# Kernel tuning notes

Hardware: AMD Instinct MI355X
Metric: run time of the kernel (lower is better)

## Reference

```python
import jax, jax.numpy as jnp
import numpy as np
import math

L, D, H, B, NT = 4, 512, 8, 128, 512
D_HID = int(D * 4.0 / 3.0)  # 682; linear0 outputs 2*D_HID for reglu
EPS = 1e-5


def layer_norm(x, g, b):
    mu = jnp.mean(x, axis=-1, keepdims=True)
    var = jnp.var(x, axis=-1, keepdims=True)
    return (x - mu) * jax.lax.rsqrt(var + EPS) * g + b


def mha(x_q, x_kv, Wq, bq, Wk, bk, Wv, bv, Wo, bo):
    q = x_q @ Wq.T + bq
    k = x_kv @ Wk.T + bk
    v = x_kv @ Wv.T + bv
    Bq, Sq, _ = q.shape
    Sk = k.shape[1]
    dh = D // H
    q = q.reshape(Bq, Sq, H, dh).transpose(0, 2, 1, 3)  # [B,H,Sq,dh]
    k = k.reshape(Bq, Sk, H, dh).transpose(0, 2, 1, 3)
    v = v.reshape(Bq, Sk, H, dh).transpose(0, 2, 1, 3)
    dots = jnp.einsum('bhqd,bhkd->bhqk', q, k) / math.sqrt(dh)
    attn = jax.nn.softmax(dots, axis=-1)
    o = jnp.einsum('bhqk,bhkd->bhqd', attn, v)
    o = o.transpose(0, 2, 1, 3).reshape(Bq, Sq, D)
    return o @ Wo.T + bo


def reglu(x):
    a, b = jnp.split(x, 2, axis=-1)
    return a * jax.nn.relu(b)


def setup_inputs() -> dict:
    key = jax.random.key(0)
    ks = iter(jax.random.split(key, 32))
    s = 0.02
    return {
        'x_num': jax.random.normal(next(ks), (B, NT, D), jnp.float32),
        'cls_w': jax.random.normal(next(ks), (1, D), jnp.float32) * s,
        'Wq': jax.random.normal(next(ks), (L, D, D), jnp.float32) * s,
        'bq': jnp.zeros((L, D), jnp.float32),
        'Wk': jax.random.normal(next(ks), (L, D, D), jnp.float32) * s,
        'bk': jnp.zeros((L, D), jnp.float32),
        'Wv': jax.random.normal(next(ks), (L, D, D), jnp.float32) * s,
        'bv': jnp.zeros((L, D), jnp.float32),
        'Wo': jax.random.normal(next(ks), (L, D, D), jnp.float32) * s,
        'bo': jnp.zeros((L, D), jnp.float32),
        'l0_w': jax.random.normal(next(ks), (L, 2 * D_HID, D), jnp.float32) * s,
        'l0_b': jnp.zeros((L, 2 * D_HID), jnp.float32),
        'l1_w': jax.random.normal(next(ks), (L, D, D_HID), jnp.float32) * s,
        'l1_b': jnp.zeros((L, D), jnp.float32),
        'n0_g': jnp.ones((L - 1, D), jnp.float32),
        'n0_b': jnp.zeros((L - 1, D), jnp.float32),
        'n1_g': jnp.ones((L, D), jnp.float32),
        'n1_b': jnp.zeros((L, D), jnp.float32),
        'ln_g': jnp.ones((D,), jnp.float32),
        'ln_b': jnp.zeros((D,), jnp.float32),
        'head_w': jax.random.normal(next(ks), (1, D), jnp.float32) * s,
        'head_b': jnp.zeros((1,), jnp.float32),
    }


def reference(x_num, cls_w, Wq, bq, Wk, bk, Wv, bv, Wo, bo,
              l0_w, l0_b, l1_w, l1_b, n0_g, n0_b, n1_g, n1_b,
              ln_g, ln_b, head_w, head_b):
    # prepend CLS token: cls_weight broadcast over batch
    x_cls = jnp.broadcast_to(cls_w[None], (x_num.shape[0], 1, D))
    x = jnp.concatenate([x_cls, x_num], axis=1)  # [B, NT+1, D]
    for i in range(L):
        is_last = i + 1 == L
        # attention block (prenormalization; layer 0 has no norm0)
        xr = layer_norm(x, n0_g[i - 1], n0_b[i - 1]) if i > 0 else x
        x_q = xr[:, :1] if is_last else xr  # last layer: query only CLS
        xr = mha(x_q, xr, Wq[i], bq[i], Wk[i], bk[i], Wv[i], bv[i], Wo[i], bo[i])
        if is_last:
            x = x[:, :1]
        x = x + xr
        # FFN block with reglu
        xr = layer_norm(x, n1_g[i], n1_b[i])
        xr = reglu(xr @ l0_w[i].T + l0_b[i])
        xr = xr @ l1_w[i].T + l1_b[i]
        x = x + xr
    x = x[:, 0]  # CLS representation [B, D]
    x = layer_norm(x, ln_g, ln_b)
    x = jax.nn.relu(x)
    x = x @ head_w.T + head_b
    return x.squeeze(-1)  # [B]
```

## Files before the change

kernel.cpp:

```cpp
#include <hip/hip_runtime.h>
#include <stdint.h>

typedef __attribute__((ext_vector_type(4))) float f32x4;
typedef __attribute__((ext_vector_type(8))) short short8;
typedef __attribute__((ext_vector_type(8))) _Float16 half8;

#define DMODEL 512
#define SEQ 513
#define BATCH 128
#define NROWS (BATCH*SEQ)
#define DHID 682
#define DHID2 1364
#define HP 768
#define QKVS 1536
#define KVB 64
#define NKT 9
#define QSF 0.1803368801111244f

__device__ __forceinline__ float h2f(ushort u){ return (float)__builtin_bit_cast(_Float16, u); }
__device__ __forceinline__ ushort f2h(float f){ return __builtin_bit_cast(ushort, (_Float16)f); }
__device__ __forceinline__ uint pk2h(float a, float b){
  return __builtin_bit_cast(uint, __builtin_amdgcn_cvt_pkrtz(a, b));
}
__device__ __forceinline__ void gload16(const void* g, void* lds){
  __builtin_amdgcn_global_load_lds((const __attribute__((address_space(1))) void*)g,
                                   (__attribute__((address_space(3))) void*)lds, 16, 0, 0);
}
__device__ __forceinline__ int xcd_wg(int orig, int nwg){
  const int q = nwg >> 3, r = nwg & 7;
  const int xcd = orig & 7, idx = orig >> 3;
  return (xcd < r) ? (xcd*(q+1) + idx) : (r*(q+1) + (xcd-r)*q + idx);
}

template<int EPI>
__global__ __launch_bounds__(256,3) void gemm_bt(
    const ushort* __restrict__ A, const ushort* __restrict__ W,
    const float* __restrict__ bias, ushort* __restrict__ Cb, float* __restrict__ Cf,
    int K, int ldc, int gx, int nwg)
{
  __shared__ char lds[32768];
  const int t = threadIdx.x, lane = t & 63, w = t >> 6;
  const int fr = lane & 15, g = lane >> 4;
  const int l7 = lane & 7, l8 = lane >> 3;
  const int wg = xcd_wg(blockIdx.x, nwg);
  const int row0 = (wg / gx) << 7;
  const int col0 = (wg % gx) << 7;
  const int wr = (w >> 1) << 6, wc = (w & 1) << 6;

  const int chunkoff = (l7 ^ l8) << 3;
  const ushort* Ag = A + (size_t)(row0 + w*8 + l8) * K + chunkoff;
  const ushort* Wg = W + (size_t)(col0 + w*8 + l8) * K + chunkoff;

  f32x4 acc[4][4] = {};

  for (int k0 = 0; k0 < K; k0 += 64) {
    __syncthreads();
#pragma unroll
    for (int p = 0; p < 4; ++p) {
      gload16(Ag + (size_t)(p*32)*K + k0, lds + p*4096 + w*1024);
      gload16(Wg + (size_t)(p*32)*K + k0, lds + 16384 + p*4096 + w*1024);
    }
    __syncthreads();
#pragma unroll
    for (int ks = 0; ks < 2; ++ks) {
      half8 af[4], wf[4];
#pragma unroll
      for (int m = 0; m < 4; ++m) {
        const int row = wr + m*16 + fr;
        af[m] = *(const half8*)(lds + row*128 + (((g + ks*4) ^ (fr & 7)) << 4));
      }
#pragma unroll
      for (int n = 0; n < 4; ++n) {
        const int row = wc + n*16 + fr;
        wf[n] = *(const half8*)(lds + 16384 + row*128 + (((g + ks*4) ^ (fr & 7)) << 4));
      }
#pragma unroll
      for (int m = 0; m < 4; ++m)
#pragma unroll
        for (int n = 0; n < 4; ++n)
          acc[m][n] = __builtin_amdgcn_mfma_f32_16x16x32_f16(af[m], wf[n], acc[m][n], 0, 0, 0);
    }
  }

  const int r0 = (lane >> 4) << 2;
#pragma unroll
  for (int m = 0; m < 4; ++m) {
    const int rg = row0 + wr + m*16 + r0;
#pragma unroll
    for (int n = 0; n < 4; ++n) {
      const int cg = col0 + wc + n*16 + fr;
      const float bi = bias[cg];
      if (EPI == 0) {
#pragma unroll
        for (int r = 0; r < 4; ++r)
          Cb[(size_t)(rg + r)*ldc + cg] = f2h(acc[m][n][r] + bi);
      } else {
#pragma unroll
        for (int r = 0; r < 4; ++r) {
          const size_t ix = (size_t)(rg + r)*ldc + cg;
          Cf[ix] += acc[m][n][r] + bi;
        }
      }
    }
  }
}

__global__ __launch_bounds__(256,2) void gemm_res_ln(
    const ushort* __restrict__ A, const ushort* __restrict__ W,
    const float* __restrict__ bias, float* __restrict__ x,
    const float* __restrict__ gamma, const float* __restrict__ beta,
    ushort* __restrict__ xb, int K)
{
  __shared__ char lds[73728];
  const int t = threadIdx.x, lane = t & 63, w = t >> 6;
  const int fr = lane & 15, g = lane >> 4;
  const int l7 = lane & 7, l8 = lane >> 3;
  const int row0 = blockIdx.x << 6;

  const int chunkoff = (l7 ^ l8) << 3;
  const ushort* Ag = A + (size_t)(row0 + w*8 + l8) * K + chunkoff;
  const ushort* Wg = W + (size_t)(w*8 + l8) * K + chunkoff;

  f32x4 acc[4][8] = {};

  for (int k0 = 0; k0 < K; k0 += 64) {
    __syncthreads();
    gload16(Ag + k0,                 lds + w*1024);
    gload16(Ag + (size_t)32*K + k0,  lds + 4096 + w*1024);
#pragma unroll
    for (int p = 0; p < 16; ++p)
      gload16(Wg + (size_t)(p*32)*K + k0, lds + 8192 + p*4096 + w*1024);
    __syncthreads();
#pragma unroll
    for (int ks = 0; ks < 2; ++ks) {
      half8 af[4], wf[8];
#pragma unroll
      for (int m = 0; m < 4; ++m) {
        const int row = m*16 + fr;
        af[m] = *(const half8*)(lds + row*128 + (((g + ks*4) ^ (fr & 7)) << 4));
      }
#pragma unroll
      for (int n = 0; n < 8; ++n) {
        const int row = (w << 7) + n*16 + fr;
        wf[n] = *(const half8*)(lds + 8192 + row*128 + (((g + ks*4) ^ (fr & 7)) << 4));
      }
#pragma unroll
      for (int m = 0; m < 4; ++m)
#pragma unroll
        for (int n = 0; n < 8; ++n)
          acc[m][n] = __builtin_amdgcn_mfma_f32_16x16x32_f16(af[m], wf[n], acc[m][n], 0, 0, 0);
    }
  }

  ushort* fb16   = (ushort*)lds;
  float2* redrow = (float2*)(lds + 66560);
  float*  gb     = (float*)(lds + 67072);

  __syncthreads();
#pragma unroll
  for (int n = 0; n < 8; ++n) {
    const int cg = (w << 7) + n*16 + fr;
    const float bi = bias[cg];
#pragma unroll
    for (int m = 0; m < 4; ++m)
#pragma unroll
      for (int r = 0; r < 4; ++r)
        fb16[(m*16 + g*4 + r)*520 + cg] = f2h(acc[m][n][r] + bi);
  }
  if (t < 128) *(f32x4*)&gb[t*4]            = *(const f32x4*)&gamma[t*4];
  else         *(f32x4*)&gb[512 + (t-128)*4] = *(const f32x4*)&beta[(t-128)*4];
  __syncthreads();

  const int q = t & 15;
  const int rbase = t >> 4;
#pragma unroll
  for (int rr = 0; rr < 4; ++rr) {
    const int row = rr*16 + rbase;
    const size_t xrow = (size_t)(row0 + row)*DMODEL;
    float ps = 0.f, pss = 0.f;
#pragma unroll
    for (int j = 0; j < 8; ++j) {
      const int c = q*4 + j*64;
      const uint2 pk = *(const uint2*)&fb16[row*520 + c];
      f32x4 v;
      v[0] = h2f((ushort)(pk.x & 0xffffu)); v[1] = h2f((ushort)(pk.x >> 16));
      v[2] = h2f((ushort)(pk.y & 0xffffu)); v[3] = h2f((ushort)(pk.y >> 16));
      const f32x4 xo = *(const f32x4*)&x[xrow + c];
      v += xo;
      *(f32x4*)&x[xrow + c] = v;
      uint2 opk; opk.x = pk2h(v[0], v[1]); opk.y = pk2h(v[2], v[3]);
      *(uint2*)&fb16[row*520 + c] = opk;
      ps  += v[0]+v[1]+v[2]+v[3];
      pss += v[0]*v[0]+v[1]*v[1]+v[2]*v[2]+v[3]*v[3];
    }
#pragma unroll
    for (int mask = 1; mask <= 8; mask <<= 1) {
      ps  += __shfl_xor(ps,  mask);
      pss += __shfl_xor(pss, mask);
    }
    if (q == 0) redrow[row] = float2{ps, pss};
  }
  __syncthreads();
#pragma unroll
  for (int rr = 0; rr < 4; ++rr) {
    const int row = rr*16 + rbase;
    const float2 sr = redrow[row];
    const float mu = sr.x * (1.f/512.f);
    const float rstd = rsqrtf(sr.y*(1.f/512.f) - mu*mu + 1e-5f);
    const size_t xbrow = (size_t)(row0 + row)*DMODEL;
#pragma unroll
    for (int j = 0; j < 8; ++j) {
      const int c = q*4 + j*64;
      const uint2 pk = *(const uint2*)&fb16[row*520 + c];
      f32x4 v;
      v[0] = h2f((ushort)(pk.x & 0xffffu)); v[1] = h2f((ushort)(pk.x >> 16));
      v[2] = h2f((ushort)(pk.y & 0xffffu)); v[3] = h2f((ushort)(pk.y >> 16));
      const f32x4 ga = *(const f32x4*)&gb[c];
      const f32x4 be = *(const f32x4*)&gb[512 + c];
      f32x4 o_;
#pragma unroll
      for (int e = 0; e < 4; ++e) o_[e] = (v[e] - mu)*rstd*ga[e] + be[e];
      uint2 u; u.x = pk2h(o_[0], o_[1]); u.y = pk2h(o_[2], o_[3]);
      *(uint2*)&xb[xbrow + c] = u;
    }
  }
}

__global__ __launch_bounds__(256,2) void gemm_ffn(
    const ushort* __restrict__ A, const ushort* __restrict__ Wa, const ushort* __restrict__ Wb,
    const float* __restrict__ ba, const float* __restrict__ bb, ushort* __restrict__ H,
    int K, int ldc, int gx, int nwg)
{
  __shared__ char lds[49152];
  const int t = threadIdx.x, lane = t & 63, w = t >> 6;
  const int fr = lane & 15, g = lane >> 4;
  const int l7 = lane & 7, l8 = lane >> 3;
  const int wg = xcd_wg(blockIdx.x, nwg);
  const int row0 = (wg / gx) << 7;
  const int col0 = (wg % gx) << 7;
  const int wr = (w >> 1) << 6, wc = (w & 1) << 6;

  const int chunkoff = (l7 ^ l8) << 3;
  const ushort* Ag  = A  + (size_t)(row0 + w*8 + l8) * K + chunkoff;
  const ushort* WaG = Wa + (size_t)(col0 + w*8 + l8) * K + chunkoff;
  const ushort* WbG = Wb + (size_t)(col0 + w*8 + l8) * K + chunkoff;

  f32x4 aa[4][4] = {}, ab[4][4] = {};

  for (int k0 = 0; k0 < K; k0 += 64) {
    __syncthreads();
#pragma unroll
    for (int p = 0; p < 4; ++p) {
      gload16(Ag  + (size_t)(p*32)*K + k0, lds + p*4096 + w*1024);
      gload16(WaG + (size_t)(p*32)*K + k0, lds + 16384 + p*4096 + w*1024);
      gload16(WbG + (size_t)(p*32)*K + k0, lds + 32768 + p*4096 + w*1024);
    }
    __syncthreads();
#pragma unroll
    for (int ks = 0; ks < 2; ++ks) {
      half8 af[4], wa[4], wb[4];
#pragma unroll
      for (int m = 0; m < 4; ++m) {
        const int row = wr + m*16 + fr;
        af[m] = *(const half8*)(lds + row*128 + (((g + ks*4) ^ (fr & 7)) << 4));
      }
#pragma unroll
      for (int n = 0; n < 4; ++n) {
        const int row = wc + n*16 + fr;
        const int off = row*128 + (((g + ks*4) ^ (fr & 7)) << 4);
        wa[n] = *(const half8*)(lds + 16384 + off);
        wb[n] = *(const half8*)(lds + 32768 + off);
      }
#pragma unroll
      for (int m = 0; m < 4; ++m)
#pragma unroll
        for (int n = 0; n < 4; ++n) {
          aa[m][n] = __builtin_amdgcn_mfma_f32_16x16x32_f16(af[m], wa[n], aa[m][n], 0, 0, 0);
          ab[m][n] = __builtin_amdgcn_mfma_f32_16x16x32_f16(af[m], wb[n], ab[m][n], 0, 0, 0);
        }
    }
  }

  const int r0 = (lane >> 4) << 2;
#pragma unroll
  for (int m = 0; m < 4; ++m) {
    const int rg = row0 + wr + m*16 + r0;
#pragma unroll
    for (int n = 0; n < 4; ++n) {
      const int cg = col0 + wc + n*16 + fr;
      const float bav = ba[cg], bbv = bb[cg];
#pragma unroll
      for (int r = 0; r < 4; ++r) {
        const float av = aa[m][n][r] + bav;
        const float bv = ab[m][n][r] + bbv;
        H[(size_t)(rg + r)*ldc + cg] = f2h(av * fmaxf(bv, 0.f));
      }
    }
  }
}

__global__ __launch_bounds__(256,4) void attn_fused(
    const ushort* __restrict__ qkv, ushort* __restrict__ o)
{
  __shared__ char lds[40960];
  const int t = threadIdx.x;

  if (blockIdx.x >= 4096) {
    const int bh = blockIdx.x - 4096;
    const int b = bh >> 3, h = bh & 7;
    float* sc   = (float*)lds;
    float* qsh  = (float*)(lds + 2112);
    float* red  = (float*)(lds + 2368);
    float* osum = (float*)(lds + 2432);
    const ushort* k = qkv + 512;
    const ushort* v = qkv + 1024;
    const ushort* qb2 = qkv + (size_t)512*QKVS;
    if (t < 64) qsh[t] = h2f(qb2[(size_t)b*SEQ*QKVS + h*64 + t]);
    __syncthreads();
    for (int key = t; key < SEQ; key += 256) {
      const ushort* kr = k + ((size_t)b*SEQ + key)*QKVS + h*64;
      float s = 0.f;
#pragma unroll 8
      for (int d = 0; d < 64; ++d) s += qsh[d]*h2f(kr[d]);
      sc[key] = s;
    }
    __syncthreads();
    float lm = -1e30f;
    for (int key = t; key < SEQ; key += 256) lm = fmaxf(lm, sc[key]);
#pragma unroll
    for (int mask=1; mask<64; mask<<=1) lm = fmaxf(lm, __shfl_xor(lm, mask));
    if ((t&63)==0) red[t>>6] = lm;
    __syncthreads();
    const float mx = fmaxf(fmaxf(red[0],red[1]), fmaxf(red[2],red[3]));
    float ls = 0.f;
    for (int key = t; key < SEQ; key += 256){ float pp = exp2f(sc[key]-mx); sc[key]=pp; ls += pp; }
#pragma unroll
    for (int mask=1; mask<64; mask<<=1) ls += __shfl_xor(ls, mask);
    if ((t&63)==0) red[4 + (t>>6)] = ls;
    __syncthreads();
    const float ssum = red[4]+red[5]+red[6]+red[7];
    const int d = t & 63, kc = t >> 6;
    float op = 0.f;
    for (int key = kc; key < SEQ; key += 4)
      op += sc[key] * h2f(v[((size_t)b*SEQ + key)*QKVS + h*64 + d]);
    osum[t] = op;
    __syncthreads();
    if (t < 64) {
      const float oo = (osum[t]+osum[64+t]+osum[128+t]+osum[192+t]) / ssum;
      o[((size_t)b*SEQ + 512)*DMODEL + h*64 + t] = f2h(oo);
    }
    return;
  }

  const int bid = blockIdx.x;
  const int sw = (bid & 7)*512 + (bid >> 3);
  const int qt = sw & 3;
  const int hb = sw >> 2;
  const int h = hb & 7, b = hb >> 3;
  const int lane = t & 63, w = t >> 6;
  const int fr = lane & 15, g = lane >> 4, gq4 = g << 2;
  const size_t rowB = (size_t)b * SEQ;
  const ushort* q = qkv;
  const ushort* k = qkv + 512;
  const ushort* v = qkv + 1024;

  char* const Ks  = lds;
  char* const Vs  = lds + 8192;
  char* const VTs = lds + 16384;
  char* const pb  = lds + 24576 + w*4096;

  const int qr0 = qt*128 + w*32;

  half8 qf[2][2];
#pragma unroll
  for (int nq = 0; nq < 2; ++nq) {
    const int qrow = qr0 + nq*16 + fr;
#pragma unroll
    for (int kk = 0; kk < 2; ++kk)
      qf[nq][kk] = *(const half8*)&q[(rowB + qrow)*QKVS + h*64 + kk*32 + g*8];
  }

  f32x4 accO[2][4] = {};
  float mrun[2] = {-1e30f, -1e30f};
  float lrun[2] = {0.f, 0.f};

  const int l8 = lane >> 3, l7 = lane & 7;
  const int chunk = l7 ^ l8;
  auto STAGE = [&](int kt2) {
#pragma unroll
    for (int i = 0; i < 2; ++i) {
      const int row = i*32 + (w<<3) + l8;
      const int keyg = min(kt2*KVB + row, 512);
      const size_t gsrc = (rowB + keyg)*QKVS + h*64 + chunk*8;
      gload16(k + gsrc, Ks + i*4096 + w*1024);
      gload16(v + gsrc, Vs + i*4096 + w*1024);
    }
  };

  const int db  = (lane & 7) | ((w & 1) << 3);
  const int kbq = l8 | ((w & 2) << 2);
  const int d0 = db << 2, key0 = kbq << 2;

  STAGE(0);

  for (int kt = 0; kt < NKT; ++kt) {
    __syncthreads();

    f32x4 sc4[4][2] = {};
    __builtin_amdgcn_s_setprio(1);
#pragma unroll
    for (int kk = 0; kk < 2; ++kk) {
      half8 kf[4];
#pragma unroll
      for (int mk = 0; mk < 4; ++mk) {
        const int row = mk*16 + fr;
        kf[mk] = *(const half8*)(Ks + row*128 + ((kk*64 + g*16) ^ ((fr&7)<<4)));
      }
#pragma unroll
      for (int mk = 0; mk < 4; ++mk)
#pragma unroll
        for (int nq = 0; nq < 2; ++nq)
          sc4[mk][nq] = __builtin_amdgcn_mfma_f32_16x16x32_f16(kf[mk], qf[nq][kk], sc4[mk][nq], 0, 0, 0);
    }
    __builtin_amdgcn_s_setprio(0);

    {
      uint2 a[4];
#pragma unroll
      for (int i = 0; i < 4; ++i) {
        const int row = key0 + i;
        a[i] = *(const uint2*)(Vs + row*128 + ((d0*2) ^ ((row&7)<<4)));
      }
      uint2 bb[4];
      bb[0].x = (a[0].x & 0xffffu) | (a[1].x << 16);
      bb[0].y = (a[2].x & 0xffffu) | (a[3].x << 16);
      bb[1].x = (a[0].x >> 16) | (a[1].x & 0xffff0000u);
      bb[1].y = (a[2].x >> 16) | (a[3].x & 0xffff0000u);
      bb[2].x = (a[0].y & 0xffffu) | (a[1].y << 16);
      bb[2].y = (a[2].y & 0xffffu) | (a[3].y << 16);
      bb[3].x = (a[0].y >> 16) | (a[1].y & 0xffff0000u);
      bb[3].y = (a[2].y >> 16) | (a[3].y & 0xffff0000u);
#pragma unroll
      for (int j = 0; j < 4; ++j) {
        const int drow = d0 + j;
        *(uint2*)(VTs + drow*128 + ((key0*2) ^ ((drow&7)<<4))) = bb[j];
      }
    }

    if (kt == NKT-1) {
#pragma unroll
      for (int mk = 0; mk < 4; ++mk)
#pragma unroll
        for (int r = 0; r < 4; ++r)
          if (mk + gq4 + r) { sc4[mk][0][r] = -1e30f; sc4[mk][1][r] = -1e30f; }
    }

    __syncthreads();

    if (kt+1 < NKT) STAGE(kt+1);

    float al2[2];
    bool resc[2];
#pragma unroll
    for (int nq = 0; nq < 2; ++nq) {
      float tm = sc4[0][nq][0];
#pragma unroll
      for (int mk = 0; mk < 4; ++mk)
#pragma unroll
        for (int r = 0; r < 4; ++r) tm = fmaxf(tm, sc4[mk][nq][r]);
      tm = fmaxf(tm, __shfl_xor(tm, 16));
      tm = fmaxf(tm, __shfl_xor(tm, 32));
      float mref;
      if (__all(tm - mrun[nq] <= 8.f)) {
        mref = mrun[nq];
        al2[nq] = 1.f; resc[nq] = false;
      } else {
        const float mnew = fmaxf(mrun[nq], tm);
        al2[nq] = exp2f(mrun[nq] - mnew);
        mrun[nq] = mnew;
        mref = mnew;
        resc[nq] = true;
      }
      float rs = 0.f;
#pragma unroll
      for (int mk = 0; mk < 4; ++mk)
#pragma unroll
        for (int r = 0; r < 4; ++r) {
          const float pv = exp2f(sc4[mk][nq][r] - mref);
          sc4[mk][nq][r] = pv;
          rs += pv;
        }
      rs += __shfl_xor(rs, 16);
      rs += __shfl_xor(rs, 32);
      lrun[nq] = resc[nq] ? (lrun[nq]*al2[nq] + rs) : (lrun[nq] + rs);
      char* prow = pb + (nq*16 + fr)*128;
#pragma unroll
      for (int mk = 0; mk < 4; ++mk) {
        uint2 pk;
        pk.x = pk2h(sc4[mk][nq][0], sc4[mk][nq][1]);
        pk.y = pk2h(sc4[mk][nq][2], sc4[mk][nq][3]);
        *(uint2*)(prow + ((mk*32 + gq4*2) ^ ((fr&7)<<4))) = pk;
      }
    }

#pragma unroll
    for (int mq = 0; mq < 2; ++mq) {
      if (resc[mq]) {
#pragma unroll
        for (int r = 0; r < 4; ++r) {
          const float alr = __shfl(al2[mq], (lane & 48) | (gq4 + r));
#pragma unroll
          for (int dn = 0; dn < 4; ++dn) accO[mq][dn][r] *= alr;
        }
      }
    }

    asm volatile("" ::: "memory");

    __builtin_amdgcn_s_setprio(1);
#pragma unroll
    for (int kk2 = 0; kk2 < 2; ++kk2) {
      half8 pf[2];
#pragma unroll
      for (int mq = 0; mq < 2; ++mq)
        pf[mq] = *(const half8*)(pb + (mq*16 + fr)*128 + ((kk2*64 + g*16) ^ ((fr&7)<<4)));
      half8 vf[4];
#pragma unroll
      for (int dn = 0; dn < 4; ++dn) {
        const int row = dn*16 + fr;
        vf[dn] = *(const half8*)(VTs + row*128 + ((kk2*64 + g*16) ^ ((fr&7)<<4)));
      }
#pragma unroll
      for (int mq = 0; mq < 2; ++mq)
#pragma unroll
        for (int dn = 0; dn < 4; ++dn)
          accO[mq][dn] = __builtin_amdgcn_mfma_f32_16x16x32_f16(pf[mq], vf[dn], accO[mq][dn], 0, 0, 0);
    }
    __builtin_amdgcn_s_setprio(0);
  }

#pragma unroll
  for (int mq = 0; mq < 2; ++mq)
#pragma unroll
    for (int r = 0; r < 4; ++r) {
      const int qrow = qr0 + mq*16 + gq4 + r;
      const float ls = __shfl(lrun[mq], (lane & 48) | (gq4 + r));
      const float inv = 1.f / ls;
#pragma unroll
      for (int dn = 0; dn < 4; ++dn)
        o[(rowB + qrow)*DMODEL + h*64 + dn*16 + fr] = f2h(accO[mq][dn][r] * inv);
    }
}

__global__ __launch_bounds__(256) void attn_cls(
    const ushort* __restrict__ qbase, size_t qstride,
    const ushort* __restrict__ qkv,
    ushort* __restrict__ obase, size_t ostride)
{
  const int bh = blockIdx.x;
  const int b = bh >> 3, h = bh & 7;
  const int t = threadIdx.x;
  __shared__ float sc[SEQ];
  __shared__ float qsh[64];
  __shared__ float red[8];
  __shared__ float osum[256];
  const ushort* k = qkv + 512;
  const ushort* v = qkv + 1024;
  if (t < 64) qsh[t] = h2f(qbase[(size_t)b*qstride + h*64 + t]);
  __syncthreads();
  for (int key = t; key < SEQ; key += 256) {
    const ushort* kr = k + ((size_t)b*SEQ + key)*QKVS + h*64;
    float s = 0.f;
#pragma unroll 8
    for (int d = 0; d < 64; ++d) s += qsh[d]*h2f(kr[d]);
    sc[key] = s;
  }
  __syncthreads();
  float lm = -1e30f;
  for (int key = t; key < SEQ; key += 256) lm = fmaxf(lm, sc[key]);
#pragma unroll
  for (int mask=1; mask<64; mask<<=1) lm = fmaxf(lm, __shfl_xor(lm, mask));
  if ((t&63)==0) red[t>>6] = lm;
  __syncthreads();
  const float mx = fmaxf(fmaxf(red[0],red[1]), fmaxf(red[2],red[3]));
  float ls = 0.f;
  for (int key = t; key < SEQ; key += 256){ float pp = exp2f(sc[key]-mx); sc[key]=pp; ls += pp; }
#pragma unroll
  for (int mask=1; mask<64; mask<<=1) ls += __shfl_xor(ls, mask);
  if ((t&63)==0) red[4 + (t>>6)] = ls;
  __syncthreads();
  const float ssum = red[4]+red[5]+red[6]+red[7];
  const int d = t & 63, kc = t >> 6;
  float op = 0.f;
  for (int key = kc; key < SEQ; key += 4)
    op += sc[key] * h2f(v[((size_t)b*SEQ + key)*QKVS + h*64 + d]);
  osum[t] = op;
  __syncthreads();
  if (t < 64) {
    const float oo = (osum[t]+osum[64+t]+osum[128+t]+osum[192+t]) / ssum;
    obase[(size_t)b*ostride + h*64 + t] = f2h(oo);
  }
}

__global__ __launch_bounds__(256) void ln_kernel(
    const float* __restrict__ x, const float* __restrict__ gamma, const float* __restrict__ beta,
    ushort* __restrict__ out, int nrows)
{
  const int row = blockIdx.x*4 + (threadIdx.x >> 6);
  const int lane = threadIdx.x & 63;
  if (row >= nrows) return;
  const float* xr = x + (size_t)row*DMODEL;
  float4 a = *(const float4*)(xr + lane*8);
  float4 b = *(const float4*)(xr + lane*8 + 4);
  float s  = a.x+a.y+a.z+a.w+b.x+b.y+b.z+b.w;
  float ss = a.x*a.x+a.y*a.y+a.z*a.z+a.w*a.w+b.x*b.x+b.y*b.y+b.z*b.z+b.w*b.w;
#pragma unroll
  for (int mask=1; mask<64; mask<<=1){ s += __shfl_xor(s,mask); ss += __shfl_xor(ss,mask); }
  const float mu = s*(1.f/512.f);
  const float rstd = rsqrtf(ss*(1.f/512.f) - mu*mu + 1e-5f);
  float vals[8] = {a.x,a.y,a.z,a.w,b.x,b.y,b.z,b.w};
  short8 pk;
#pragma unroll
  for (int j=0;j<8;++j){
    const int c = lane*8 + j;
    pk[j] = (short)f2h((vals[j]-mu)*rstd*gamma[c] + beta[c]);
  }
  *(short8*)(out + (size_t)row*DMODEL + lane*8) = pk;
}

__global__ void embed_kernel(const float* __restrict__ x_num, const float* __restrict__ cls_w,
                             float* __restrict__ x, ushort* __restrict__ xb)
{
  const size_t i = (size_t)blockIdx.x*256 + threadIdx.x;
  if (i >= (size_t)NROWS*128) return;
  const int row = (int)(i >> 7);
  const int c4 = ((int)(i & 127)) << 2;
  const int b = row / SEQ;
  const int s = row - b*SEQ;
  float4 val;
  if (s == 0) val = *(const float4*)(cls_w + c4);
  else        val = *(const float4*)(x_num + ((size_t)b*512 + (s-1))*512 + c4);
  *(float4*)(x + (size_t)row*DMODEL + c4) = val;
  ushort4 pk;
  pk.x = f2h(val.x); pk.y = f2h(val.y); pk.z = f2h(val.z); pk.w = f2h(val.w);
  *(ushort4*)(xb + (size_t)row*DMODEL + c4) = pk;
}

__global__ void convert_pad(const float* __restrict__ in, ushort* __restrict__ out,
                            int R, int C, int RP, int CP, int layers, float scale,
                            int r0, int srcRL, size_t ostride)
{
  const size_t i = (size_t)blockIdx.x*256 + threadIdx.x;
  const size_t per = (size_t)RP*CP;
  if (i >= per*layers) return;
  const int l = (int)(i / per);
  const int rem = (int)(i - (size_t)l*per);
  const int r = rem / CP;
  const int c = rem - r*CP;
  ushort val = 0;
  if (r < R && c < C) val = f2h(in[((size_t)l*srcRL + r0 + r)*C + c] * scale);
  out[(size_t)l*ostride + (size_t)r*CP + c] = val;
}

__global__ void build_bias(const float* __restrict__ bq, const float* __restrict__ bk,
                           const float* __restrict__ bv, const float* __restrict__ l0b,
                           float* __restrict__ fqkv, float* __restrict__ fa, float* __restrict__ fb)
{
  const int i = blockIdx.x*256 + threadIdx.x;
  if (i < 4*1536) {
    const int l = i / 1536, j = i - l*1536;
    float val;
    if (j < 512)       val = bq[l*512 + j] * QSF;
    else if (j < 1024) val = bk[l*512 + j - 512];
    else               val = bv[l*512 + j - 1024];
    fqkv[i] = val;
  }
  if (i < 4*HP) {
    const int l = i / HP, j = i - l*HP;
    fa[i] = (j < DHID) ? l0b[l*DHID2 + j] : 0.f;
    fb[i] = (j < DHID) ? l0b[l*DHID2 + DHID + j] : 0.f;
  }
}

__global__ void gather_cls(const ushort* __restrict__ xb, const float* __restrict__ x,
                           ushort* __restrict__ xq, float* __restrict__ xc)
{
  const int b = blockIdx.x, lane = threadIdx.x;
  const size_t src = (size_t)b*SEQ*DMODEL;
  *(short8*)(xq + b*DMODEL + lane*8) = *(const short8*)(xb + src + lane*8);
  *(float4*)(xc + b*DMODEL + lane*8)     = *(const float4*)(x + src + lane*8);
  *(float4*)(xc + b*DMODEL + lane*8 + 4) = *(const float4*)(x + src + lane*8 + 4);
}

__global__ void head_kernel(const float* __restrict__ xc, const float* __restrict__ g,
                            const float* __restrict__ be, const float* __restrict__ hw,
                            const float* __restrict__ hb, float* __restrict__ out)
{
  const int row = blockIdx.x;
  const int lane = threadIdx.x;
  const float* xr = xc + (size_t)row*DMODEL;
  float4 a = *(const float4*)(xr + lane*8);
  float4 b = *(const float4*)(xr + lane*8 + 4);
  float s  = a.x+a.y+a.z+a.w+b.x+b.y+b.z+b.w;
  float ss = a.x*a.x+a.y*a.y+a.z*a.z+a.w*a.w+b.x*b.x+b.y*b.y+b.z*b.z+b.w*b.w;
#pragma unroll
  for (int mask=1; mask<64; mask<<=1){ s += __shfl_xor(s,mask); ss += __shfl_xor(ss,mask); }
  const float mu = s*(1.f/512.f);
  const float rstd = rsqrtf(ss*(1.f/512.f) - mu*mu + 1e-5f);
  float vals[8] = {a.x,a.y,a.z,a.w,b.x,b.y,b.z,b.w};
  float acc = 0.f;
#pragma unroll
  for (int j=0;j<8;++j){
    const int c = lane*8 + j;
    float tv = (vals[j]-mu)*rstd*g[c] + be[c];
    acc += fmaxf(tv, 0.f) * hw[c];
  }
#pragma unroll
  for (int mask=1; mask<64; mask<<=1) acc += __shfl_xor(acc, mask);
  if (lane==0) out[row] = acc + hb[0];
}

extern "C" void kernel_launch(void* const* d_in, const int* in_sizes, int n_in,
                              void* d_out, int out_size, void* d_ws, size_t ws_size,
                              hipStream_t stream)
{
  const float* x_num = (const float*)d_in[0];
  const float* cls_w = (const float*)d_in[1];
  const float* Wq = (const float*)d_in[2];
  const float* bq = (const float*)d_in[3];
  const float* Wk = (const float*)d_in[4];
  const float* bk = (const float*)d_in[5];
  const float* Wv = (const float*)d_in[6];
  const float* bv = (const float*)d_in[7];
  const float* Wo = (const float*)d_in[8];
  const float* bo = (const float*)d_in[9];
  const float* l0_w = (const float*)d_in[10];
  const float* l0_b = (const float*)d_in[11];
  const float* l1_w = (const float*)d_in[12];
  const float* l1_b = (const float*)d_in[13];
  const float* n0_g = (const float*)d_in[14];
  const float* n0_b = (const float*)d_in[15];
  const float* n1_g = (const float*)d_in[16];
  const float* n1_b = (const float*)d_in[17];
  const float* ln_g = (const float*)d_in[18];
  const float* ln_b = (const float*)d_in[19];
  const float* head_w = (const float*)d_in[20];
  const float* head_b = (const float*)d_in[21];
  float* out = (float*)d_out;

  char* p = (char*)d_ws;
  auto alloc = [&](size_t bytes){ char* r = p; p += (bytes + 255) & ~(size_t)255; return r; };

  float* x  = (float*)alloc((size_t)NROWS*DMODEL*4);
  char* U   = alloc((size_t)NROWS*DMODEL*2);
  ushort* xb = (ushort*)U;
  ushort* ob = (ushort*)U;
  char* QKVG = alloc((size_t)NROWS*QKVS*2);
  ushort* qkv = (ushort*)QKVG;
  ushort* hbuf = (ushort*)QKVG;
  ushort* wqkvb = (ushort*)alloc((size_t)4*QKVS*512*2);
  ushort* wob  = (ushort*)alloc((size_t)4*512*512*2);
  ushort* wl0a = (ushort*)alloc((size_t)4*HP*512*2);
  ushort* wl0b = (ushort*)alloc((size_t)4*HP*512*2);
  ushort* l1wp = (ushort*)alloc((size_t)4*512*HP*2);
  float*  fqkvb = (float*)alloc((size_t)4*QKVS*4);
  float*  l0ba = (float*)alloc((size_t)4*HP*4);
  float*  l0bb = (float*)alloc((size_t)4*HP*4);
  ushort* xq_cls = (ushort*)alloc(128*512*2);
  float*  xcf = (float*)alloc(128*512*4);
  ushort* qc = (ushort*)alloc(128*512*2);
  ushort* oc = (ushort*)alloc(128*512*2);
  ushort* hc = (ushort*)alloc((size_t)128*HP*2);
  ushort* xcb = (ushort*)alloc(128*512*2);

  auto cdiv = [](size_t a, size_t b){ return (unsigned)((a + b - 1)/b); };

  convert_pad<<<cdiv((size_t)4*512*512,256),256,0,stream>>>(Wq, wqkvb,            512,512,512,512,4, QSF, 0, 512, (size_t)QKVS*512);
  convert_pad<<<cdiv((size_t)4*512*512,256),256,0,stream>>>(Wk, wqkvb + 512*512,  512,512,512,512,4, 1.f, 0, 512, (size_t)QKVS*512);
  convert_pad<<<cdiv((size_t)4*512*512,256),256,0,stream>>>(Wv, wqkvb + 1024*512, 512,512,512,512,4, 1.f, 0, 512, (size_t)QKVS*512);
  convert_pad<<<cdiv((size_t)4*512*512,256),256,0,stream>>>(Wo, wob, 512,512,512,512,4, 1.f, 0, 512, (size_t)512*512);
  convert_pad<<<cdiv((size_t)4*HP*512,256),256,0,stream>>>(l0_w, wl0a, DHID,512,HP,512,4, 1.f, 0,    DHID2, (size_t)HP*512);
  convert_pad<<<cdiv((size_t)4*HP*512,256),256,0,stream>>>(l0_w, wl0b, DHID,512,HP,512,4, 1.f, DHID, DHID2, (size_t)HP*512);
  convert_pad<<<cdiv((size_t)4*512*HP,256),256,0,stream>>>(l1_w, l1wp, 512,DHID,512,HP,4, 1.f, 0, 512, (size_t)512*HP);
  build_bias<<<cdiv(4*QKVS,256),256,0,stream>>>(bq, bk, bv, l0_b, fqkvb, l0ba, l0bb);

  embed_kernel<<<cdiv((size_t)NROWS*128,256),256,0,stream>>>(x_num, cls_w, x, xb);

  const int nwQKV = 12*513, nwF = 6*513, nwKV = 8*513;
  const int nRL = NROWS/64;
  for (int i = 0; i < 3; ++i) {
    gemm_bt<0><<<nwQKV,256,0,stream>>>(xb, wqkvb+(size_t)i*QKVS*512, fqkvb+(size_t)i*QKVS, qkv, nullptr, 512, QKVS, 12, nwQKV);
    attn_fused<<<5120,256,0,stream>>>(qkv, ob);
    gemm_res_ln<<<nRL,256,0,stream>>>(ob, wob+(size_t)i*262144, bo+i*512, x,
                                      n1_g+(size_t)i*512, n1_b+(size_t)i*512, xb, 512);
    gemm_ffn<<<nwF,256,0,stream>>>(xb, wl0a+(size_t)i*HP*512, wl0b+(size_t)i*HP*512,
                                   l0ba+(size_t)i*HP, l0bb+(size_t)i*HP, hbuf, 512, HP, 6, nwF);
    gemm_res_ln<<<nRL,256,0,stream>>>(hbuf, l1wp+(size_t)i*512*HP, l1_b+i*512, x,
                                      n0_g+(size_t)i*512, n0_b+(size_t)i*512, xb, HP);
  }

  gather_cls<<<128,64,0,stream>>>(xb, x, xq_cls, xcf);
  gemm_bt<0><<<4,256,0,stream>>>(xq_cls, wqkvb+(size_t)3*QKVS*512, fqkvb+(size_t)3*QKVS, qc, nullptr, 512, 512, 4, 4);
  gemm_bt<0><<<nwKV,256,0,stream>>>(xb, wqkvb+(size_t)3*QKVS*512 + 512*512, fqkvb+(size_t)3*QKVS + 512,
                                    qkv + 512, nullptr, 512, QKVS, 8, nwKV);
  attn_cls<<<1024,256,0,stream>>>(qc, 512, qkv, oc, 512);
  gemm_bt<1><<<4,256,0,stream>>>(oc, wob+(size_t)3*262144, bo+3*512, nullptr, xcf, 512, 512, 4, 4);
  ln_kernel<<<cdiv(128,4),256,0,stream>>>(xcf, n1_g+3*512, n1_b+3*512, xcb, 128);
  gemm_ffn<<<6,256,0,stream>>>(xcb, wl0a+(size_t)3*HP*512, wl0b+(size_t)3*HP*512,
                               l0ba+(size_t)3*HP, l0bb+(size_t)3*HP, hc, 512, HP, 6, 6);
  gemm_bt<1><<<4,256,0,stream>>>(hc, l1wp+(size_t)3*512*HP, l1_b+3*512, nullptr, xcf, HP, 512, 4, 4);
  head_kernel<<<128,64,0,stream>>>(xcf, ln_g, ln_b, head_w, head_b, out);
}
```

Before: 2.380 ms.

## Double attention block size to 8 waves sharing each K/V tile

The fused attention kernel now runs 512 threads per block, covering 256 query rows instead of 128, so each staged K/V tile and its transpose serve twice as many queries and global K/V traffic per head halves. Staging and the V transpose are rewritten so each thread handles a single 16-byte chunk or a 2x4 sub-block. The CLS-row tail path is adjusted for 8 waves. LDS grows to 56KB per block with launch bounds of 2 blocks per CU, which cuts occupancy and the number of blocks.

```diff
diff --git a/kernel.cpp b/kernel.cpp
--- a/kernel.cpp
+++ b/kernel.cpp
@@ -299,14 +299,14 @@
   }
 }
 
-__global__ __launch_bounds__(256,4) void attn_fused(
+__global__ __launch_bounds__(512,2) void attn_fused(
     const ushort* __restrict__ qkv, ushort* __restrict__ o)
 {
-  __shared__ char lds[40960];
+  __shared__ char lds[57344];
   const int t = threadIdx.x;
 
-  if (blockIdx.x >= 4096) {
-    const int bh = blockIdx.x - 4096;
+  if (blockIdx.x >= 2048) {
+    const int bh = blockIdx.x - 2048;
     const int b = bh >> 3, h = bh & 7;
     float* sc   = (float*)lds;
     float* qsh  = (float*)(lds + 2112);
@@ -317,7 +317,7 @@
     const ushort* qb2 = qkv + (size_t)512*QKVS;
     if (t < 64) qsh[t] = h2f(qb2[(size_t)b*SEQ*QKVS + h*64 + t]);
     __syncthreads();
-    for (int key = t; key < SEQ; key += 256) {
+    for (int key = t; key < SEQ; key += 512) {
       const ushort* kr = k + ((size_t)b*SEQ + key)*QKVS + h*64;
       float s = 0.f;
 #pragma unroll 8
@@ -326,36 +326,42 @@
     }
     __syncthreads();
     float lm = -1e30f;
-    for (int key = t; key < SEQ; key += 256) lm = fmaxf(lm, sc[key]);
+    for (int key = t; key < SEQ; key += 512) lm = fmaxf(lm, sc[key]);
 #pragma unroll
     for (int mask=1; mask<64; mask<<=1) lm = fmaxf(lm, __shfl_xor(lm, mask));
     if ((t&63)==0) red[t>>6] = lm;
     __syncthreads();
-    const float mx = fmaxf(fmaxf(red[0],red[1]), fmaxf(red[2],red[3]));
+    float mx = red[0];
+#pragma unroll
+    for (int i2 = 1; i2 < 8; ++i2) mx = fmaxf(mx, red[i2]);
     float ls = 0.f;
-    for (int key = t; key < SEQ; key += 256){ float pp = exp2f(sc[key]-mx); sc[key]=pp; ls += pp; }
+    for (int key = t; key < SEQ; key += 512){ float pp = exp2f(sc[key]-mx); sc[key]=pp; ls += pp; }
 #pragma unroll
     for (int mask=1; mask<64; mask<<=1) ls += __shfl_xor(ls, mask);
-    if ((t&63)==0) red[4 + (t>>6)] = ls;
-    __syncthreads();
-    const float ssum = red[4]+red[5]+red[6]+red[7];
+    if ((t&63)==0) red[8 + (t>>6)] = ls;
+    __syncthreads();
+    float ssum = red[8];
+#pragma unroll
+    for (int i2 = 1; i2 < 8; ++i2) ssum += red[8 + i2];
     const int d = t & 63, kc = t >> 6;
     float op = 0.f;
-    for (int key = kc; key < SEQ; key += 4)
+    for (int key = kc; key < SEQ; key += 8)
       op += sc[key] * h2f(v[((size_t)b*SEQ + key)*QKVS + h*64 + d]);
     osum[t] = op;
     __syncthreads();
     if (t < 64) {
-      const float oo = (osum[t]+osum[64+t]+osum[128+t]+osum[192+t]) / ssum;
-      o[((size_t)b*SEQ + 512)*DMODEL + h*64 + t] = f2h(oo);
+      float oo = 0.f;
+#pragma unroll
+      for (int i2 = 0; i2 < 8; ++i2) oo += osum[t + i2*64];
+      o[((size_t)b*SEQ + 512)*DMODEL + h*64 + t] = f2h(oo / ssum);
     }
     return;
   }
 
   const int bid = blockIdx.x;
-  const int sw = (bid & 7)*512 + (bid >> 3);
-  const int qt = sw & 3;
-  const int hb = sw >> 2;
+  const int sw = (bid & 7)*256 + (bid >> 3);
+  const int qt = sw & 1;
+  const int hb = sw >> 1;
   const int h = hb & 7, b = hb >> 3;
   const int lane = t & 63, w = t >> 6;
   const int fr = lane & 15, g = lane >> 4, gq4 = g << 2;
@@ -369,7 +375,7 @@
   char* const VTs = lds + 16384;
   char* const pb  = lds + 24576 + w*4096;
 
-  const int qr0 = qt*128 + w*32;
+  const int qr0 = qt*256 + w*32;
 
   half8 qf[2][2];
 #pragma unroll
@@ -384,22 +390,17 @@
   float mrun[2] = {-1e30f, -1e30f};
   float lrun[2] = {0.f, 0.f};
 
-  const int l8 = lane >> 3, l7 = lane & 7;
-  const int chunk = l7 ^ l8;
+  const int srowS = t >> 3, sslot = t & 7;
+  const int chunkS = sslot ^ (srowS & 7);
   auto STAGE = [&](int kt2) {
-#pragma unroll
-    for (int i = 0; i < 2; ++i) {
-      const int row = i*32 + (w<<3) + l8;
-      const int keyg = min(kt2*KVB + row, 512);
-      const size_t gsrc = (rowB + keyg)*QKVS + h*64 + chunk*8;
-      gload16(k + gsrc, Ks + i*4096 + w*1024);
-      gload16(v + gsrc, Vs + i*4096 + w*1024);
-    }
+    const int keyg = min(kt2*KVB + srowS, 512);
+    const size_t gsrc = (rowB + keyg)*QKVS + h*64 + chunkS*8;
+    gload16(k + gsrc, Ks + t*16);
+    gload16(v + gsrc, Vs + t*16);
   };
 
-  const int db  = (lane & 7) | ((w & 1) << 3);
-  const int kbq = l8 | ((w & 2) << 2);
-  const int d0 = db << 2, key0 = kbq << 2;
+  const int td0 = (t & 15) << 2;
+  const int tk0 = (t >> 4) << 1;
 
   STAGE(0);
 
@@ -425,25 +426,17 @@
     __builtin_amdgcn_s_setprio(0);
 
     {
-      uint2 a[4];
-#pragma unroll
-      for (int i = 0; i < 4; ++i) {
-        const int row = key0 + i;
-        a[i] = *(const uint2*)(Vs + row*128 + ((d0*2) ^ ((row&7)<<4)));
-      }
-      uint2 bb[4];
-      bb[0].x = (a[0].x & 0xffffu) | (a[1].x << 16);
-      bb[0].y = (a[2].x & 0xffffu) | (a[3].x << 16);
-      bb[1].x = (a[0].x >> 16) | (a[1].x & 0xffff0000u);
-      bb[1].y = (a[2].x >> 16) | (a[3].x & 0xffff0000u);
-      bb[2].x = (a[0].y & 0xffffu) | (a[1].y << 16);
-      bb[2].y = (a[2].y & 0xffffu) | (a[3].y << 16);
-      bb[3].x = (a[0].y >> 16) | (a[1].y & 0xffff0000u);
-      bb[3].y = (a[2].y >> 16) | (a[3].y & 0xffff0000u);
+      const uint2 a0 = *(const uint2*)(Vs + tk0*128     + ((td0*2) ^ ((tk0&7)<<4)));
+      const uint2 a1 = *(const uint2*)(Vs + (tk0+1)*128 + ((td0*2) ^ (((tk0+1)&7)<<4)));
+      uint vals[4];
+      vals[0] = (a0.x & 0xffffu) | (a1.x << 16);
+      vals[1] = (a0.x >> 16)     | (a1.x & 0xffff0000u);
+      vals[2] = (a0.y & 0xffffu) | (a1.y << 16);
+      vals[3] = (a0.y >> 16)     | (a1.y & 0xffff0000u);
 #pragma unroll
       for (int j = 0; j < 4; ++j) {
-        const int drow = d0 + j;
-        *(uint2*)(VTs + drow*128 + ((key0*2) ^ ((drow&7)<<4))) = bb[j];
+        const int drow = td0 + j;
+        *(uint*)(VTs + drow*128 + ((tk0*2) ^ ((drow&7)<<4))) = vals[j];
       }
     }
 
@@ -790,7 +783,7 @@
   const int nRL = NROWS/64;
   for (int i = 0; i < 3; ++i) {
     gemm_bt<0><<<nwQKV,256,0,stream>>>(xb, wqkvb+(size_t)i*QKVS*512, fqkvb+(size_t)i*QKVS, qkv, nullptr, 512, QKVS, 12, nwQKV);
-    attn_fused<<<5120,256,0,stream>>>(qkv, ob);
+    attn_fused<<<3072,512,0,stream>>>(qkv, ob);
     gemm_res_ln<<<nRL,256,0,stream>>>(ob, wob+(size_t)i*262144, bo+i*512, x,
                                       n1_g+(size_t)i*512, n1_b+(size_t)i*512, xb, 512);
     gemm_ffn<<<nwF,256,0,stream>>>(xb, wl0a+(size_t)i*HP*512, wl0b+(size_t)i*HP*512,
```

Result: slower. 2.579 ms (+8.4%).
